# Kernel tuning notes

Measured on AMD Instinct MI355X. Metric: run time of the kernel, lower is better.

## Reference

```python
import jax, jax.numpy as jnp
import numpy as np

N, C, K2 = 40000, 128, 9  # active voxels, channels, 3x3 kernel taps
HEAD_OUT = {"hm": 3, "center": 2, "center_z": 1, "dim": 3, "rot": 2}
EPS = 1e-5
INIT_BIAS = -2.66


def setup_inputs() -> dict:
    key = jax.random.key(0)
    ks = jax.random.split(key, 16)
    feats = jax.random.normal(ks[0], (N, C), dtype=jnp.float32)
    # precomputed submanifold-conv neighbor indices (one per kernel tap, all valid)
    nbr_idx = jax.random.randint(ks[1], (N, K2), 0, N, dtype=jnp.int32)
    H = len(HEAD_OUT)
    inp = {"feats": feats, "nbr_idx": nbr_idx}
    # stacked 3x3 SubMConv weights for all heads (kaiming-ish scale)
    inp["W1"] = jax.random.normal(ks[2], (H, K2, C, C), dtype=jnp.float32) * (2.0 / (K2 * C)) ** 0.5
    inp["gamma"] = jnp.ones((H, C), jnp.float32)
    inp["beta"] = jnp.zeros((H, C), jnp.float32)
    for i, (name, oc) in enumerate(HEAD_OUT.items()):
        inp[f"w_{name}"] = jax.random.normal(ks[3 + i], (C, oc), dtype=jnp.float32) * (2.0 / C) ** 0.5
        inp[f"b_{name}"] = (jnp.full((oc,), INIT_BIAS, jnp.float32) if name == "hm"
                             else jnp.zeros((oc,), jnp.float32))
    return inp


def reference(feats, nbr_idx, W1, gamma, beta,
              w_hm, b_hm, w_center, b_center, w_center_z, b_center_z,
              w_dim, b_dim, w_rot, b_rot):
    # SubMConv2d as gather + contraction over kernel taps (shared by all heads)
    gathered = feats[nbr_idx]                       # [N, K2, C]
    y = jnp.einsum('nkc,hkcd->hnd', gathered, W1)   # [H, N, C]
    # BatchNorm1d (training-mode forward: biased batch stats over voxels) + ReLU
    mean = y.mean(axis=1, keepdims=True)
    var = y.var(axis=1, keepdims=True)
    y = jax.nn.relu((y - mean) * jax.lax.rsqrt(var + EPS) * gamma[:, None, :] + beta[:, None, :])
    # per-head 1x1 SubMConv with bias
    heads = [(w_hm, b_hm), (w_center, b_center), (w_center_z, b_center_z),
             (w_dim, b_dim), (w_rot, b_rot)]
    outs = [y[i] @ w + b for i, (w, b) in enumerate(heads)]
    # concat head outputs along channel: [N, 3+2+1+3+2] = [N, 11]
    return jnp.concatenate(outs, axis=-1)
```

## Files before the change

### kernel.cpp

```cpp
#include <hip/hip_runtime.h>
#include <stdint.h>

#define NVOX 40000
#define CCH  128
#define K2   9
#define NH   5
#define TILES 313

typedef __attribute__((ext_vector_type(8))) short bf16x8;
typedef __attribute__((ext_vector_type(4))) float f32x4;

__device__ __forceinline__ unsigned short f2b(float f) {
  union { float f; unsigned int u; } v; v.f = f;
  return (unsigned short)((v.u + 0x7fffu + ((v.u >> 16) & 1u)) >> 16);
}
__device__ __forceinline__ float b2f(unsigned short u) {
  union { unsigned int u; float f; } v; v.u = ((unsigned int)u) << 16;
  return v.f;
}
__device__ __forceinline__ void g2l16(const void* g, void* l) {
  __builtin_amdgcn_global_load_lds(
      (const __attribute__((address_space(1))) unsigned int*)g,
      (__attribute__((address_space(3))) unsigned int*)l, 16, 0, 0);
}
__device__ __forceinline__ int swz(int row, int col) {
  return row * 128 + ((((col >> 3) ^ (row & 15)) << 3) | (col & 7));
}

__global__ void prep(const float4* __restrict__ feats, ushort4* __restrict__ fb,
                     const float* __restrict__ w1, unsigned short* __restrict__ w1t,
                     float* __restrict__ sums) {
  __shared__ unsigned short t[128 * 34];
  int b = blockIdx.x;
  if (b < 5000) {
    int i = b * 256 + threadIdx.x;
    if (i < NVOX * CCH / 4) {
      float4 v = feats[i];
      ushort4 r;
      r.x = f2b(v.x); r.y = f2b(v.y); r.z = f2b(v.z); r.w = f2b(v.w);
      fb[i] = r;
    }
    return;
  }
  if (b == 5180) {
    for (int i = threadIdx.x; i < 2 * NH * CCH; i += 256) sums[i] = 0.f;
    return;
  }
  int bb = b - 5000;
  int tile = bb >> 2;
  int q = bb & 3;
  const float* src = w1 + (size_t)tile * 16384 + q * 32 * 128;
  for (int e = threadIdx.x; e < 4096; e += 256) {
    int c = e >> 7, d = e & 127;
    t[d * 34 + c] = f2b(src[e]);
  }
  __syncthreads();
  unsigned short* dst = w1t + (size_t)tile * 16384 + q * 32;
  for (int e = threadIdx.x; e < 4096; e += 256) {
    int d = e >> 5, c = e & 31;
    dst[d * 128 + c] = t[d * 34 + c];
  }
}

__device__ __forceinline__ void stageBhalf(unsigned short* dst, const unsigned short* wp,
                                           int half, int wave, int lane) {
  int lrow = lane >> 3;
  int lch  = lane & 7;
#pragma unroll
  for (int i = 0; i < 4; ++i) {
    int rb = (wave * 4 + i) * 8;
    g2l16(wp + (rb + lrow) * 128 + half * 64 + ((lch ^ lrow) << 3),
          &dst[(wave * 4 + i) * 512]);
  }
}

__global__ void __launch_bounds__(256, 4) conv_gemm(
    const unsigned short* __restrict__ fb,
    const int* __restrict__ nbr,
    const unsigned short* __restrict__ w1t,
    unsigned short* __restrict__ yb,
    float* __restrict__ sums)
{
  __shared__ __align__(16) unsigned short Bsb[2][64 * 128];
  __shared__ int idxs[128 * K2];

  const int bid = blockIdx.x;
  const int s = bid / 40;
  const int r = bid % 40;
  const int h = r >> 3;
  const int x = r & 7;
  const int tile = s * 8 + x;
  if (tile >= TILES) return;
  const int n0 = tile * 128;

  const int tid = threadIdx.x;
  const int wave = tid >> 6;
  const int lane = tid & 63;
  const int m = lane & 15;
  const int quad = lane >> 4;

  const unsigned short* wh = w1t + ((size_t)h * K2 << 14);

  stageBhalf(Bsb[0], wh, 0, wave, lane);

  for (int i = tid; i < 128 * K2; i += 256) {
    int rr = i / K2;
    int gn = n0 + rr; if (gn > NVOX - 1) gn = NVOX - 1;
    idxs[i] = nbr[gn * K2 + (i - rr * K2)];
  }
  __syncthreads();

  bf16x8 A[2][2][4];
  {
    int i0 = idxs[(wave * 32 + m) * K2 + 0];
    int i1 = idxs[(wave * 32 + 16 + m) * K2 + 0];
    const unsigned short* p0 = fb + (size_t)i0 * CCH + quad * 8;
    const unsigned short* p1 = fb + (size_t)i1 * CCH + quad * 8;
#pragma unroll
    for (int kc = 0; kc < 4; ++kc) {
      A[0][0][kc] = *(const bf16x8*)(p0 + kc * 32);
      A[0][1][kc] = *(const bf16x8*)(p1 + kc * 32);
    }
  }
  asm volatile("s_waitcnt vmcnt(0)" ::: "memory");
  __syncthreads();

  f32x4 acc[2][8] = {};

#pragma unroll
  for (int k = 0; k < K2; ++k) {
    const int par = k & 1;

    stageBhalf(Bsb[1], wh + ((size_t)k << 14), 1, wave, lane);
    if (k + 1 < K2) {
      int i0 = idxs[(wave * 32 + m) * K2 + k + 1];
      int i1 = idxs[(wave * 32 + 16 + m) * K2 + k + 1];
      const unsigned short* p0 = fb + (size_t)i0 * CCH + quad * 8;
      const unsigned short* p1 = fb + (size_t)i1 * CCH + quad * 8;
#pragma unroll
      for (int kc = 0; kc < 4; ++kc) {
        A[par ^ 1][0][kc] = *(const bf16x8*)(p0 + kc * 32);
        A[par ^ 1][1][kc] = *(const bf16x8*)(p1 + kc * 32);
      }
    }
#pragma unroll
    for (int kc = 0; kc < 2; ++kc) {
      bf16x8 bfr[8];
#pragma unroll
      for (int ni = 0; ni < 8; ++ni)
        bfr[ni] = *(const bf16x8*)&Bsb[0][(ni * 16 + m) * 64 + ((((kc & 1) * 4 + quad) ^ (m & 7)) << 3)];
#pragma unroll
      for (int ni = 0; ni < 8; ++ni) {
        acc[0][ni] = __builtin_amdgcn_mfma_f32_16x16x32_bf16(A[par][0][kc], bfr[ni], acc[0][ni], 0, 0, 0);
        acc[1][ni] = __builtin_amdgcn_mfma_f32_16x16x32_bf16(A[par][1][kc], bfr[ni], acc[1][ni], 0, 0, 0);
      }
    }
    asm volatile("s_waitcnt vmcnt(0)" ::: "memory");
    __syncthreads();

    if (k + 1 < K2)
      stageBhalf(Bsb[0], wh + ((size_t)(k + 1) << 14), 0, wave, lane);
#pragma unroll
    for (int kc = 2; kc < 4; ++kc) {
      bf16x8 bfr[8];
#pragma unroll
      for (int ni = 0; ni < 8; ++ni)
        bfr[ni] = *(const bf16x8*)&Bsb[1][(ni * 16 + m) * 64 + ((((kc & 1) * 4 + quad) ^ (m & 7)) << 3)];
#pragma unroll
      for (int ni = 0; ni < 8; ++ni) {
        acc[0][ni] = __builtin_amdgcn_mfma_f32_16x16x32_bf16(A[par][0][kc], bfr[ni], acc[0][ni], 0, 0, 0);
        acc[1][ni] = __builtin_amdgcn_mfma_f32_16x16x32_bf16(A[par][1][kc], bfr[ni], acc[1][ni], 0, 0, 0);
      }
    }
    asm volatile("s_waitcnt vmcnt(0)" ::: "memory");
    __syncthreads();
  }

  const bool full = (n0 + 128 <= NVOX);
  unsigned short* epi = &Bsb[0][0];

#pragma unroll
  for (int mi = 0; mi < 2; ++mi)
#pragma unroll
    for (int ni = 0; ni < 8; ++ni)
#pragma unroll
      for (int rr = 0; rr < 4; ++rr) {
        int row = wave * 32 + mi * 16 + quad * 4 + rr;
        int col = ni * 16 + m;
        epi[swz(row, col)] = f2b(acc[mi][ni][rr]);
      }

  float psm[8], pq[8];
#pragma unroll
  for (int ni = 0; ni < 8; ++ni) {
    float sm = 0.f, q = 0.f;
#pragma unroll
    for (int mi = 0; mi < 2; ++mi)
#pragma unroll
      for (int rr = 0; rr < 4; ++rr) {
        float v = acc[mi][ni][rr];
        if (!full && n0 + wave * 32 + mi * 16 + quad * 4 + rr >= NVOX) v = 0.f;
        sm += v; q += v * v;
      }
    psm[ni] = sm; pq[ni] = q;
  }
  __syncthreads();

  for (int i = tid; i < 2048; i += 256) {
    int row = i >> 4;
    int c = i & 15;
    if (n0 + row < NVOX)
      *(bf16x8*)(yb + ((size_t)h * NVOX + n0 + row) * CCH + c * 8) =
          *(const bf16x8*)&epi[row * 128 + ((c ^ (row & 15)) << 3)];
  }
  __syncthreads();

  float2* pb = (float2*)&Bsb[0][0];
#pragma unroll
  for (int ni = 0; ni < 8; ++ni)
    pb[(ni * 16 + m) * 17 + wave * 4 + quad] = make_float2(psm[ni], pq[ni]);
  __syncthreads();

  if (tid < 128) {
    float sm = 0.f, q = 0.f;
#pragma unroll
    for (int c = 0; c < 16; ++c) {
      float2 p = pb[tid * 17 + c];
      sm += p.x; q += p.y;
    }
    atomicAdd(&sums[h * CCH + tid], sm);
    atomicAdd(&sums[NH * CCH + h * CCH + tid], q);
  }
}

__global__ void __launch_bounds__(256) head_fuse(
    const unsigned short* __restrict__ yb, const float* __restrict__ sums,
    const float* __restrict__ gamma, const float* __restrict__ beta,
    const float* __restrict__ w_hm, const float* __restrict__ b_hm,
    const float* __restrict__ w_ce, const float* __restrict__ b_ce,
    const float* __restrict__ w_cz, const float* __restrict__ b_cz,
    const float* __restrict__ w_dm, const float* __restrict__ b_dm,
    const float* __restrict__ w_rt, const float* __restrict__ b_rt,
    float* __restrict__ out)
{
  __shared__ unsigned short t[64 * 128];
  __shared__ float pbuf[4][64][12];
  __shared__ float scl[NH * CCH], shf[NH * CCH];

  const int tid = threadIdx.x;
  const int v0 = blockIdx.x * 64;
  const int vx = tid & 63;
  const int qd = tid >> 6;

  for (int i = tid; i < NH * CCH; i += 256) {
    float mean = sums[i] * (1.f / NVOX);
    float var = sums[NH * CCH + i] * (1.f / NVOX) - mean * mean;
    float rstd = rsqrtf(var + 1e-5f);
    float sc = rstd * gamma[i];
    scl[i] = sc;
    shf[i] = beta[i] - mean * sc;
  }

  float part[11];
#pragma unroll
  for (int j = 0; j < 11; ++j) part[j] = 0.f;

#pragma unroll
  for (int h = 0; h < NH; ++h) {
    __syncthreads();
#pragma unroll
    for (int i = 0; i < 4; ++i) {
      int idx = i * 256 + tid;
      int row = idx >> 4, c = idx & 15;
      *(bf16x8*)&t[row * 128 + ((c ^ (row & 15)) << 3)] =
          *(const bf16x8*)(yb + ((size_t)h * NVOX + v0 + row) * CCH + c * 8);
    }
    __syncthreads();

    const float* sc = scl + h * CCH;
    const float* sh = shf + h * CCH;
    const float* wp; int oc, off;
    switch (h) {
      case 0: wp = w_hm; oc = 3; off = 0; break;
      case 1: wp = w_ce; oc = 2; off = 3; break;
      case 2: wp = w_cz; oc = 1; off = 5; break;
      case 3: wp = w_dm; oc = 3; off = 6; break;
      default: wp = w_rt; oc = 2; off = 9; break;
    }
#pragma unroll
    for (int qq = 0; qq < 4; ++qq) {
      int q8 = qd * 4 + qq;
      bf16x8 pk = *(const bf16x8*)&t[vx * 128 + ((q8 ^ (vx & 15)) << 3)];
#pragma unroll
      for (int e = 0; e < 8; ++e) {
        int d = q8 * 8 + e;
        float z = fmaf(b2f((unsigned short)pk[e]), sc[d], sh[d]);
        z = fmaxf(z, 0.f);
        const float* wr = wp + d * oc;
        part[off] = fmaf(z, wr[0], part[off]);
        if (oc > 1) part[off + 1] = fmaf(z, wr[1], part[off + 1]);
        if (oc > 2) part[off + 2] = fmaf(z, wr[2], part[off + 2]);
      }
    }
  }

#pragma unroll
  for (int j = 0; j < 11; ++j) pbuf[qd][vx][j] = part[j];
  __syncthreads();
  if (tid < 64) {
    float o[11];
#pragma unroll
    for (int j = 0; j < 11; ++j)
      o[j] = pbuf[0][tid][j] + pbuf[1][tid][j] + pbuf[2][tid][j] + pbuf[3][tid][j];
    o[0] += b_hm[0]; o[1] += b_hm[1]; o[2] += b_hm[2];
    o[3] += b_ce[0]; o[4] += b_ce[1];
    o[5] += b_cz[0];
    o[6] += b_dm[0]; o[7] += b_dm[1]; o[8] += b_dm[2];
    o[9] += b_rt[0]; o[10] += b_rt[1];
    float* op = out + (size_t)(v0 + tid) * 11;
#pragma unroll
    for (int j = 0; j < 11; ++j) op[j] = o[j];
  }
}

extern "C" void kernel_launch(void* const* d_in, const int* in_sizes, int n_in,
                              void* d_out, int out_size, void* d_ws, size_t ws_size,
                              hipStream_t stream) {
  const float* feats = (const float*)d_in[0];
  const int*   nbr   = (const int*)d_in[1];
  const float* W1    = (const float*)d_in[2];
  const float* gamma = (const float*)d_in[3];
  const float* beta  = (const float*)d_in[4];
  const float* w_hm = (const float*)d_in[5];  const float* b_hm = (const float*)d_in[6];
  const float* w_ce = (const float*)d_in[7];  const float* b_ce = (const float*)d_in[8];
  const float* w_cz = (const float*)d_in[9];  const float* b_cz = (const float*)d_in[10];
  const float* w_dm = (const float*)d_in[11]; const float* b_dm = (const float*)d_in[12];
  const float* w_rt = (const float*)d_in[13]; const float* b_rt = (const float*)d_in[14];
  float* out = (float*)d_out;

  char* ws = (char*)d_ws;
  unsigned short* w1t = (unsigned short*)ws;
  unsigned short* fb  = (unsigned short*)(ws + 11796480);
  unsigned short* yb  = (unsigned short*)(ws + 22036480);
  float* sums = (float*)(ws + 73236480);

  prep<<<5181, 256, 0, stream>>>((const float4*)feats, (ushort4*)fb, W1, w1t, sums);
  conv_gemm<<<1600, 256, 0, stream>>>(fb, nbr, w1t, yb, sums);
  head_fuse<<<625, 256, 0, stream>>>(yb, sums, gamma, beta, w_hm, b_hm, w_ce, b_ce,
                                     w_cz, b_cz, w_dm, b_dm, w_rt, b_rt, out);
}
```

Before: 259.4 us.

## Use 8 waves per conv tile with 16 rows each, split weight-transpose blocks

conv_gemm now runs 512 threads per block, with each wave owning 16 output rows instead of 32. This halves the A-fragment and accumulator registers per thread and doubles the waves per tile to hide gather latency. The per-wave B-staging load count and the epilogue stats reduction (now shuffles plus an 8-way LDS reduce) are adjusted to match. prep splits each weight-transpose block in two, giving more, smaller blocks. The trade-off is more LDS reads of B per MFMA, since each B fragment feeds only one MFMA instead of two, and 512-thread blocks with launch_bounds(512,4) may constrain registers.

```diff
diff --git a/kernel.cpp b/kernel.cpp
--- a/kernel.cpp
+++ b/kernel.cpp
@@ -30,7 +30,7 @@
 __global__ void prep(const float4* __restrict__ feats, ushort4* __restrict__ fb,
                      const float* __restrict__ w1, unsigned short* __restrict__ w1t,
                      float* __restrict__ sums) {
-  __shared__ unsigned short t[128 * 34];
+  __shared__ unsigned short t[64 * 34];
   int b = blockIdx.x;
   if (b < 5000) {
     int i = b * 256 + threadIdx.x;
@@ -42,39 +42,40 @@
     }
     return;
   }
-  if (b == 5180) {
+  if (b == 5360) {
     for (int i = threadIdx.x; i < 2 * NH * CCH; i += 256) sums[i] = 0.f;
     return;
   }
   int bb = b - 5000;
-  int tile = bb >> 2;
-  int q = bb & 3;
-  const float* src = w1 + (size_t)tile * 16384 + q * 32 * 128;
-  for (int e = threadIdx.x; e < 4096; e += 256) {
-    int c = e >> 7, d = e & 127;
-    t[d * 34 + c] = f2b(src[e]);
+  int tile = bb >> 3;
+  int q = (bb >> 1) & 3;
+  int dh = bb & 1;
+  const float* src = w1 + (size_t)tile * 16384 + q * 32 * 128 + dh * 64;
+  for (int e = threadIdx.x; e < 2048; e += 256) {
+    int c = e >> 6, dd = e & 63;
+    t[dd * 34 + c] = f2b(src[c * 128 + dd]);
   }
   __syncthreads();
   unsigned short* dst = w1t + (size_t)tile * 16384 + q * 32;
-  for (int e = threadIdx.x; e < 4096; e += 256) {
+  for (int e = threadIdx.x; e < 2048; e += 256) {
     int d = e >> 5, c = e & 31;
-    dst[d * 128 + c] = t[d * 34 + c];
-  }
-}
-
-__device__ __forceinline__ void stageBhalf(unsigned short* dst, const unsigned short* wp,
-                                           int half, int wave, int lane) {
+    dst[(dh * 64 + d) * 128 + c] = t[d * 34 + c];
+  }
+}
+
+__device__ __forceinline__ void stageBhalf8(unsigned short* dst, const unsigned short* wp,
+                                            int half, int wave, int lane) {
   int lrow = lane >> 3;
   int lch  = lane & 7;
 #pragma unroll
-  for (int i = 0; i < 4; ++i) {
-    int rb = (wave * 4 + i) * 8;
-    g2l16(wp + (rb + lrow) * 128 + half * 64 + ((lch ^ lrow) << 3),
-          &dst[(wave * 4 + i) * 512]);
-  }
-}
-
-__global__ void __launch_bounds__(256, 4) conv_gemm(
+  for (int i = 0; i < 2; ++i) {
+    int blk = wave * 2 + i;
+    g2l16(wp + (blk * 8 + lrow) * 128 + half * 64 + ((lch ^ lrow) << 3),
+          &dst[blk * 512]);
+  }
+}
+
+__global__ void __launch_bounds__(512, 4) conv_gemm(
     const unsigned short* __restrict__ fb,
     const int* __restrict__ nbr,
     const unsigned short* __restrict__ w1t,
@@ -101,47 +102,39 @@
 
   const unsigned short* wh = w1t + ((size_t)h * K2 << 14);
 
-  stageBhalf(Bsb[0], wh, 0, wave, lane);
-
-  for (int i = tid; i < 128 * K2; i += 256) {
+  stageBhalf8(Bsb[0], wh, 0, wave, lane);
+
+  for (int i = tid; i < 128 * K2; i += 512) {
     int rr = i / K2;
     int gn = n0 + rr; if (gn > NVOX - 1) gn = NVOX - 1;
     idxs[i] = nbr[gn * K2 + (i - rr * K2)];
   }
   __syncthreads();
 
-  bf16x8 A[2][2][4];
+  bf16x8 A[2][4];
   {
-    int i0 = idxs[(wave * 32 + m) * K2 + 0];
-    int i1 = idxs[(wave * 32 + 16 + m) * K2 + 0];
+    int i0 = idxs[(wave * 16 + m) * K2 + 0];
     const unsigned short* p0 = fb + (size_t)i0 * CCH + quad * 8;
-    const unsigned short* p1 = fb + (size_t)i1 * CCH + quad * 8;
-#pragma unroll
-    for (int kc = 0; kc < 4; ++kc) {
-      A[0][0][kc] = *(const bf16x8*)(p0 + kc * 32);
-      A[0][1][kc] = *(const bf16x8*)(p1 + kc * 32);
-    }
+#pragma unroll
+    for (int kc = 0; kc < 4; ++kc)
+      A[0][kc] = *(const bf16x8*)(p0 + kc * 32);
   }
   asm volatile("s_waitcnt vmcnt(0)" ::: "memory");
   __syncthreads();
 
-  f32x4 acc[2][8] = {};
+  f32x4 acc[8] = {};
 
 #pragma unroll
   for (int k = 0; k < K2; ++k) {
     const int par = k & 1;
 
-    stageBhalf(Bsb[1], wh + ((size_t)k << 14), 1, wave, lane);
+    stageBhalf8(Bsb[1], wh + ((size_t)k << 14), 1, wave, lane);
     if (k + 1 < K2) {
-      int i0 = idxs[(wave * 32 + m) * K2 + k + 1];
-      int i1 = idxs[(wave * 32 + 16 + m) * K2 + k + 1];
+      int i0 = idxs[(wave * 16 + m) * K2 + k + 1];
       const unsigned short* p0 = fb + (size_t)i0 * CCH + quad * 8;
-      const unsigned short* p1 = fb + (size_t)i1 * CCH + quad * 8;
-#pragma unroll
-      for (int kc = 0; kc < 4; ++kc) {
-        A[par ^ 1][0][kc] = *(const bf16x8*)(p0 + kc * 32);
-        A[par ^ 1][1][kc] = *(const bf16x8*)(p1 + kc * 32);
-      }
+#pragma unroll
+      for (int kc = 0; kc < 4; ++kc)
+        A[par ^ 1][kc] = *(const bf16x8*)(p0 + kc * 32);
     }
 #pragma unroll
     for (int kc = 0; kc < 2; ++kc) {
@@ -150,16 +143,14 @@
       for (int ni = 0; ni < 8; ++ni)
         bfr[ni] = *(const bf16x8*)&Bsb[0][(ni * 16 + m) * 64 + ((((kc & 1) * 4 + quad) ^ (m & 7)) << 3)];
 #pragma unroll
-      for (int ni = 0; ni < 8; ++ni) {
-        acc[0][ni] = __builtin_amdgcn_mfma_f32_16x16x32_bf16(A[par][0][kc], bfr[ni], acc[0][ni], 0, 0, 0);
-        acc[1][ni] = __builtin_amdgcn_mfma_f32_16x16x32_bf16(A[par][1][kc], bfr[ni], acc[1][ni], 0, 0, 0);
-      }
+      for (int ni = 0; ni < 8; ++ni)
+        acc[ni] = __builtin_amdgcn_mfma_f32_16x16x32_bf16(A[par][kc], bfr[ni], acc[ni], 0, 0, 0);
     }
     asm volatile("s_waitcnt vmcnt(0)" ::: "memory");
     __syncthreads();
 
     if (k + 1 < K2)
-      stageBhalf(Bsb[0], wh + ((size_t)(k + 1) << 14), 0, wave, lane);
+      stageBhalf8(Bsb[0], wh + ((size_t)(k + 1) << 14), 0, wave, lane);
 #pragma unroll
     for (int kc = 2; kc < 4; ++kc) {
       bf16x8 bfr[8];
@@ -167,10 +158,8 @@
       for (int ni = 0; ni < 8; ++ni)
         bfr[ni] = *(const bf16x8*)&Bsb[1][(ni * 16 + m) * 64 + ((((kc & 1) * 4 + quad) ^ (m & 7)) << 3)];
 #pragma unroll
-      for (int ni = 0; ni < 8; ++ni) {
-        acc[0][ni] = __builtin_amdgcn_mfma_f32_16x16x32_bf16(A[par][0][kc], bfr[ni], acc[0][ni], 0, 0, 0);
-        acc[1][ni] = __builtin_amdgcn_mfma_f32_16x16x32_bf16(A[par][1][kc], bfr[ni], acc[1][ni], 0, 0, 0);
-      }
+      for (int ni = 0; ni < 8; ++ni)
+        acc[ni] = __builtin_amdgcn_mfma_f32_16x16x32_bf16(A[par][kc], bfr[ni], acc[ni], 0, 0, 0);
     }
     asm volatile("s_waitcnt vmcnt(0)" ::: "memory");
     __syncthreads();
@@ -180,33 +169,31 @@
   unsigned short* epi = &Bsb[0][0];
 
 #pragma unroll
-  for (int mi = 0; mi < 2; ++mi)
-#pragma unroll
-    for (int ni = 0; ni < 8; ++ni)
-#pragma unroll
-      for (int rr = 0; rr < 4; ++rr) {
-        int row = wave * 32 + mi * 16 + quad * 4 + rr;
-        int col = ni * 16 + m;
-        epi[swz(row, col)] = f2b(acc[mi][ni][rr]);
-      }
+  for (int ni = 0; ni < 8; ++ni)
+#pragma unroll
+    for (int rr = 0; rr < 4; ++rr) {
+      int row = wave * 16 + quad * 4 + rr;
+      int col = ni * 16 + m;
+      epi[swz(row, col)] = f2b(acc[ni][rr]);
+    }
 
   float psm[8], pq[8];
 #pragma unroll
   for (int ni = 0; ni < 8; ++ni) {
     float sm = 0.f, q = 0.f;
 #pragma unroll
-    for (int mi = 0; mi < 2; ++mi)
-#pragma unroll
-      for (int rr = 0; rr < 4; ++rr) {
-        float v = acc[mi][ni][rr];
-        if (!full && n0 + wave * 32 + mi * 16 + quad * 4 + rr >= NVOX) v = 0.f;
-        sm += v; q += v * v;
-      }
+    for (int rr = 0; rr < 4; ++rr) {
+      float v = acc[ni][rr];
+      if (!full && n0 + wave * 16 + quad * 4 + rr >= NVOX) v = 0.f;
+      sm += v; q += v * v;
+    }
+    sm += __shfl_xor(sm, 16); q += __shfl_xor(q, 16);
+    sm += __shfl_xor(sm, 32); q += __shfl_xor(q, 32);
     psm[ni] = sm; pq[ni] = q;
   }
   __syncthreads();
 
-  for (int i = tid; i < 2048; i += 256) {
+  for (int i = tid; i < 2048; i += 512) {
     int row = i >> 4;
     int c = i & 15;
     if (n0 + row < NVOX)
@@ -216,16 +203,17 @@
   __syncthreads();
 
   float2* pb = (float2*)&Bsb[0][0];
-#pragma unroll
-  for (int ni = 0; ni < 8; ++ni)
-    pb[(ni * 16 + m) * 17 + wave * 4 + quad] = make_float2(psm[ni], pq[ni]);
+  if (quad == 0)
+#pragma unroll
+    for (int ni = 0; ni < 8; ++ni)
+      pb[(ni * 16 + m) * 9 + wave] = make_float2(psm[ni], pq[ni]);
   __syncthreads();
 
   if (tid < 128) {
     float sm = 0.f, q = 0.f;
 #pragma unroll
-    for (int c = 0; c < 16; ++c) {
-      float2 p = pb[tid * 17 + c];
+    for (int c = 0; c < 8; ++c) {
+      float2 p = pb[tid * 9 + c];
       sm += p.x; q += p.y;
     }
     atomicAdd(&sums[h * CCH + tid], sm);
@@ -344,8 +332,8 @@
   unsigned short* yb  = (unsigned short*)(ws + 22036480);
   float* sums = (float*)(ws + 73236480);
 
-  prep<<<5181, 256, 0, stream>>>((const float4*)feats, (ushort4*)fb, W1, w1t, sums);
-  conv_gemm<<<1600, 256, 0, stream>>>(fb, nbr, w1t, yb, sums);
+  prep<<<5361, 256, 0, stream>>>((const float4*)feats, (ushort4*)fb, W1, w1t, sums);
+  conv_gemm<<<1600, 512, 0, stream>>>(fb, nbr, w1t, yb, sums);
   head_fuse<<<625, 256, 0, stream>>>(yb, sums, gamma, beta, w_hm, b_hm, w_ce, b_ce,
                                      w_cz, b_cz, w_dm, b_dm, w_rt, b_rt, out);
 }
```

New measurement: 241.3 us. -7.0%, faster.
